# Performance work log

Measured on AMD Instinct MI355X. Metric: run time of the kernel, lower is better.

Reference implementation:

```python
import jax, jax.numpy as jnp
import numpy as np

N_CELL, N_TISSUE, H, NH = 200000, 2000, 256, 8
HD = H // NH
SCALE = HD ** -0.5
EPS = 1e-5


def _layernorm(x, g, b):
    m = jnp.mean(x, axis=-1, keepdims=True)
    v = jnp.mean((x - m) ** 2, axis=-1, keepdims=True)
    return (x - m) / jnp.sqrt(v + EPS) * g + b


def setup_inputs() -> dict:
    key = jax.random.key(0)
    ks = jax.random.split(key, 12)
    s = 0.02

    def lin(k):
        k1, k2 = jax.random.split(k)
        return (jax.random.normal(k1, (H, H), jnp.float32) * s,
                jax.random.normal(k2, (H,), jnp.float32) * s)

    Wq_bu, bq_bu = lin(ks[0])
    Wk_bu, bk_bu = lin(ks[1])
    Wv_bu, bv_bu = lin(ks[2])
    Wo_bu, bo_bu = lin(ks[3])
    Wv_td, bv_td = lin(ks[4])
    Wo_td, bo_td = lin(ks[5])
    return dict(
        cell_features=jax.random.normal(ks[6], (N_CELL, H), jnp.float32),
        tissue_features=jax.random.normal(ks[7], (N_TISSUE, H), jnp.float32),
        cluster_labels=jax.random.randint(ks[8], (N_CELL,), 0, N_TISSUE, dtype=jnp.int32),
        tissue_batch=jnp.zeros((N_TISSUE,), jnp.int32),
        Wq_bu=Wq_bu, bq_bu=bq_bu, Wk_bu=Wk_bu, bk_bu=bk_bu,
        Wv_bu=Wv_bu, bv_bu=bv_bu, Wo_bu=Wo_bu, bo_bu=bo_bu,
        Wv_td=Wv_td, bv_td=bv_td, Wo_td=Wo_td, bo_td=bo_td,
        ln_cell_g=jnp.ones((H,), jnp.float32), ln_cell_b=jnp.zeros((H,), jnp.float32),
        ln_tissue_g=jnp.ones((H,), jnp.float32), ln_tissue_b=jnp.zeros((H,), jnp.float32),
    )


def reference(cell_features, tissue_features, cluster_labels, tissue_batch,
              Wq_bu, bq_bu, Wk_bu, bk_bu, Wv_bu, bv_bu, Wo_bu, bo_bu,
              Wv_td, bv_td, Wo_td, bo_td,
              ln_cell_g, ln_cell_b, ln_tissue_g, ln_tissue_b):
    Nc = cell_features.shape[0]
    Nt = tissue_features.shape[0]

    # ---- bottom-up: each tissue node (1 query) attends over its cells (segment attention) ----
    Q = (tissue_features @ Wq_bu + bq_bu).reshape(Nt, NH, HD)   # [Nt, h, d]
    K = (cell_features @ Wk_bu + bk_bu).reshape(Nc, NH, HD)     # [Nc, h, d]
    V = (cell_features @ Wv_bu + bv_bu).reshape(Nc, NH, HD)     # [Nc, h, d]

    # per-cell score against its own cluster's tissue query
    scores = jnp.einsum('nhd,nhd->nh', K, Q[cluster_labels]) * SCALE  # [Nc, h]
    smax = jax.lax.stop_gradient(
        jax.ops.segment_max(scores, cluster_labels, num_segments=Nt))  # [Nt, h]
    ex = jnp.exp(scores - smax[cluster_labels])
    denom = jax.ops.segment_sum(ex, cluster_labels, num_segments=Nt)   # [Nt, h]
    w = ex / denom[cluster_labels]                                     # [Nc, h]
    attended = jax.ops.segment_sum(w[..., None] * V, cluster_labels,
                                   num_segments=Nt)                    # [Nt, h, d]
    attended = attended.reshape(Nt, H) @ Wo_bu + bo_bu

    counts = jax.ops.segment_sum(jnp.ones((Nc,), cell_features.dtype),
                                 cluster_labels, num_segments=Nt)
    tissue_updated = jnp.where(counts[:, None] > 0, attended, tissue_features)

    # ---- top-down: each cell attends to its single tissue token ----
    # softmax over a single key is identically 1, so q/k projections cancel:
    # attended_cell = out_proj(v_proj(tissue_updated[cluster]))
    td_per_tissue = (tissue_updated @ Wv_td + bv_td) @ Wo_td + bo_td   # [Nt, H]
    cell_updated = td_per_tissue[cluster_labels]                       # [Nc, H]

    cell_out = _layernorm(cell_features + cell_updated, ln_cell_g, ln_cell_b)
    tissue_out = _layernorm(tissue_features + tissue_updated, ln_tissue_g, ln_tissue_b)
    return (cell_out, tissue_out)
```

## Files before the change

### kernel.cpp

```cpp
#include <hip/hip_runtime.h>
#include <math.h>

#define NC 200000
#define NT 2000
#define HH 256
#define NH_ 8
#define SCALE 0.17677669529663687f
#define EPS 1e-5f
#define SLICE 128
#define PSLICES (NT + NC / SLICE + 1)
#define PSTRIDE 2056


__global__ void k_hist(const int* __restrict__ labels, int* __restrict__ counts) {
  int i = blockIdx.x * 256 + threadIdx.x;
  if (i < NC) atomicAdd(&counts[labels[i]], 1);
}

__global__ void k_scan(const int* __restrict__ counts, int* __restrict__ offsets,
                       int* __restrict__ soff, int* __restrict__ slice_t) {
  int tid = threadIdx.x;
  int base = tid * 32;
  int la[32], lb[32], scnt[32];
  int sa = 0, sb = 0;
  #pragma unroll
  for (int k = 0; k < 32; k++) {
    int idx = base + k;
    int v = (idx < NT) ? counts[idx] : 0;
    la[k] = sa; lb[k] = sb;
    scnt[k] = (v + SLICE - 1) / SLICE;
    sa += v; sb += scnt[k];
  }
  int ia_ = sa, ib_ = sb;
  #pragma unroll
  for (int d = 1; d < 64; d <<= 1) {
    int oa = __shfl_up(ia_, d, 64);
    int ob = __shfl_up(ib_, d, 64);
    if (tid >= d) { ia_ += oa; ib_ += ob; }
  }
  int ea = ia_ - sa, eb = ib_ - sb;
  #pragma unroll
  for (int k = 0; k < 32; k++) {
    int idx = base + k;
    if (idx < NT) {
      offsets[idx] = ea + la[k];
      soff[idx] = eb + lb[k];
      int st = eb + lb[k];
      for (int s2 = 0; s2 < scnt[k]; s2++) slice_t[st + s2] = idx;
    }
  }
  if (tid == 63) { offsets[NT] = ia_; soff[NT] = ib_; }
}

__global__ void k_scatter(const int* __restrict__ labels, const int* __restrict__ offsets,
                          int* __restrict__ cursor, int* __restrict__ cindex) {
  int i = blockIdx.x * 256 + threadIdx.x;
  if (i < NC) {
    int c = labels[i];
    int pos = offsets[c] + atomicAdd(&cursor[c], 1);
    cindex[pos] = i;
  }
}


__global__ __launch_bounds__(256) void k_gemm_bias(
    const float* __restrict__ A, const float* __restrict__ W,
    const float* __restrict__ bias, float* __restrict__ C, int M)
{
  __shared__ float Al[16][33];
  __shared__ float Wl[32][HH];
  int tid = threadIdx.x;
  int r0 = blockIdx.x * 16;
  float acc[16];
  #pragma unroll
  for (int r = 0; r < 16; r++) acc[r] = 0.f;
  for (int k0 = 0; k0 < HH; k0 += 32) {
    for (int e = tid; e < 16 * 32; e += 256) {
      int r = e >> 5, k = e & 31;
      int row = r0 + r;
      Al[r][k] = (row < M) ? A[(size_t)row * HH + k0 + k] : 0.f;
    }
    for (int e = tid; e < 32 * HH; e += 256) {
      int k = e >> 8, j = e & 255;
      Wl[k][j] = W[(size_t)(k0 + k) * HH + j];
    }
    __syncthreads();
    for (int k = 0; k < 32; k++) {
      float w = Wl[k][tid];
      #pragma unroll
      for (int r = 0; r < 16; r++) acc[r] += Al[r][k] * w;
    }
    __syncthreads();
  }
  float bj = bias[tid];
  #pragma unroll
  for (int r = 0; r < 16; r++) {
    int row = r0 + r;
    if (row < M) C[(size_t)row * HH + tid] = acc[r] + bj;
  }
}


__global__ __launch_bounds__(256) void k_qproj(
    const float* __restrict__ Q, const float* __restrict__ Wk,
    const float* __restrict__ bk, float* __restrict__ Qproj,
    float* __restrict__ bkq)
{
  __shared__ float Al[64][33];
  __shared__ float Bl[32][257];
  int h = blockIdx.x & 7, tb = blockIdx.x >> 3;
  int t0 = tb * 64;
  int tid = threadIdx.x;
  for (int e = tid; e < 64 * 32; e += 256) {
    int r = e >> 5, d = e & 31;
    int t = t0 + r;
    Al[r][d] = (t < NT) ? Q[(size_t)t * HH + h * 32 + d] * SCALE : 0.f;
  }
  for (int e = tid; e < 256 * 32; e += 256) {
    int j = e >> 5, d = e & 31;
    Bl[d][j] = Wk[(size_t)j * HH + h * 32 + d];
  }
  __syncthreads();
  float acc[64];
  #pragma unroll
  for (int r = 0; r < 64; r++) acc[r] = 0.f;
  for (int d = 0; d < 32; d++) {
    float b = Bl[d][tid];
    #pragma unroll
    for (int r = 0; r < 64; r++) acc[r] += Al[r][d] * b;
  }
  for (int r = 0; r < 64; r++) {
    int t = t0 + r;
    if (t < NT) Qproj[((size_t)t * NH_ + h) * HH + tid] = acc[r];
  }
  if (tid < 64) {
    int t = t0 + tid;
    if (t < NT) {
      float s = 0.f;
      #pragma unroll
      for (int d = 0; d < 32; d++) s += Al[tid][d] * bk[h * 32 + d];
      bkq[t * NH_ + h] = s;
    }
  }
}


#define GRP 4
#define ROWF 260

__global__ __launch_bounds__(256) void k_cellslice(
    const float* __restrict__ cell, const int* __restrict__ cindex,
    const int* __restrict__ offsets, const int* __restrict__ soff,
    const int* __restrict__ slice_t,
    const float* __restrict__ Qproj, const float* __restrict__ bkq,
    float* __restrict__ Pbuf)
{
  __shared__ int   cidx[SLICE];
  __shared__ float xbuf[4][GRP][ROWF];
  __shared__ float cwlds[NH_][HH];
  __shared__ float red[4][NH_];

  int s = blockIdx.x;
  if (s >= soff[NT]) return;
  int t = slice_t[s];
  int l = s - soff[t];
  int c0 = offsets[t] + l * SLICE;
  int c1 = min(c0 + SLICE, offsets[t + 1]);
  int nc = c1 - c0;

  int tid = threadIdx.x;
  int w = tid >> 6, lane = tid & 63;
  int hg = lane & 3, kc = lane >> 2;

  if (tid < SLICE) cidx[tid] = cindex[min(c0 + tid, c1 - 1)];

  const float* qpb = Qproj + (size_t)t * NH_ * HH;
  float4 qp0[4], qp1[4];
  #pragma unroll
  for (int i = 0; i < 4; i++) {
    qp0[i] = *reinterpret_cast<const float4*>(qpb + (2 * hg) * HH + (i * 16 + kc) * 4);
    qp1[i] = *reinterpret_cast<const float4*>(qpb + (2 * hg + 1) * HH + (i * 16 + kc) * 4);
  }
  float bq0 = bkq[t * NH_ + 2 * hg];
  float bq1 = bkq[t * NH_ + 2 * hg + 1];

  float4 cw0[4], cw1[4];
  #pragma unroll
  for (int i = 0; i < 4; i++) {
    cw0[i] = make_float4(0.f, 0.f, 0.f, 0.f);
    cw1[i] = make_float4(0.f, 0.f, 0.f, 0.f);
  }
  float d0 = 0.f, d1 = 0.f;

  __syncthreads();

  float (*myx)[ROWF] = xbuf[w];
  int base = w * GRP;
  float4 st[GRP];

  #pragma unroll
  for (int r = 0; r < GRP; r++)
    st[r] = *reinterpret_cast<const float4*>(
        &cell[(size_t)cidx[min(base + r, nc - 1)] * HH + lane * 4]);
  #pragma unroll
  for (int r = 0; r < GRP; r++)
    *reinterpret_cast<float4*>(&myx[r][lane * 4]) = st[r];

  for (int gb = base; gb < nc; gb += 16) {
    int gn = gb + 16;
    bool more = gn < nc;
    if (more) {
      #pragma unroll
      for (int r = 0; r < GRP; r++)
        st[r] = *reinterpret_cast<const float4*>(
            &cell[(size_t)cidx[min(gn + r, nc - 1)] * HH + lane * 4]);
    }
    #pragma unroll
    for (int c = 0; c < GRP; c++) {
      float4 x0 = *reinterpret_cast<float4*>(&myx[c][(0 * 16 + kc) * 4]);
      float4 x1 = *reinterpret_cast<float4*>(&myx[c][(1 * 16 + kc) * 4]);
      float4 x2 = *reinterpret_cast<float4*>(&myx[c][(2 * 16 + kc) * 4]);
      float4 x3 = *reinterpret_cast<float4*>(&myx[c][(3 * 16 + kc) * 4]);
      float s0 = x0.x * qp0[0].x + x0.y * qp0[0].y + x0.z * qp0[0].z + x0.w * qp0[0].w
               + x1.x * qp0[1].x + x1.y * qp0[1].y + x1.z * qp0[1].z + x1.w * qp0[1].w
               + x2.x * qp0[2].x + x2.y * qp0[2].y + x2.z * qp0[2].z + x2.w * qp0[2].w
               + x3.x * qp0[3].x + x3.y * qp0[3].y + x3.z * qp0[3].z + x3.w * qp0[3].w;
      float s1 = x0.x * qp1[0].x + x0.y * qp1[0].y + x0.z * qp1[0].z + x0.w * qp1[0].w
               + x1.x * qp1[1].x + x1.y * qp1[1].y + x1.z * qp1[1].z + x1.w * qp1[1].w
               + x2.x * qp1[2].x + x2.y * qp1[2].y + x2.z * qp1[2].z + x2.w * qp1[2].w
               + x3.x * qp1[3].x + x3.y * qp1[3].y + x3.z * qp1[3].z + x3.w * qp1[3].w;
      #pragma unroll
      for (int d = 4; d < 64; d <<= 1) {
        s0 += __shfl_xor(s0, d, 64);
        s1 += __shfl_xor(s1, d, 64);
      }
      float e0 = __expf(s0 + bq0);
      float e1 = __expf(s1 + bq1);
      if (gb + c >= nc) { e0 = 0.f; e1 = 0.f; }
      d0 += e0; d1 += e1;
      cw0[0].x += e0 * x0.x; cw0[0].y += e0 * x0.y; cw0[0].z += e0 * x0.z; cw0[0].w += e0 * x0.w;
      cw0[1].x += e0 * x1.x; cw0[1].y += e0 * x1.y; cw0[1].z += e0 * x1.z; cw0[1].w += e0 * x1.w;
      cw0[2].x += e0 * x2.x; cw0[2].y += e0 * x2.y; cw0[2].z += e0 * x2.z; cw0[2].w += e0 * x2.w;
      cw0[3].x += e0 * x3.x; cw0[3].y += e0 * x3.y; cw0[3].z += e0 * x3.z; cw0[3].w += e0 * x3.w;
      cw1[0].x += e1 * x0.x; cw1[0].y += e1 * x0.y; cw1[0].z += e1 * x0.z; cw1[0].w += e1 * x0.w;
      cw1[1].x += e1 * x1.x; cw1[1].y += e1 * x1.y; cw1[1].z += e1 * x1.z; cw1[1].w += e1 * x1.w;
      cw1[2].x += e1 * x2.x; cw1[2].y += e1 * x2.y; cw1[2].z += e1 * x2.z; cw1[2].w += e1 * x2.w;
      cw1[3].x += e1 * x3.x; cw1[3].y += e1 * x3.y; cw1[3].z += e1 * x3.z; cw1[3].w += e1 * x3.w;
    }
    if (more) {
      #pragma unroll
      for (int r = 0; r < GRP; r++)
        *reinterpret_cast<float4*>(&myx[r][lane * 4]) = st[r];
    }
  }

  if (w == 0) {
    #pragma unroll
    for (int i = 0; i < 4; i++) {
      *reinterpret_cast<float4*>(&cwlds[2 * hg][(i * 16 + kc) * 4]) = cw0[i];
      *reinterpret_cast<float4*>(&cwlds[2 * hg + 1][(i * 16 + kc) * 4]) = cw1[i];
    }
  }
  if (kc == 0) { red[w][2 * hg] = d0; red[w][2 * hg + 1] = d1; }
  __syncthreads();
  #pragma unroll
  for (int ww = 1; ww < 4; ww++) {
    if (w == ww) {
      #pragma unroll
      for (int i = 0; i < 4; i++) {
        float4 a = *reinterpret_cast<float4*>(&cwlds[2 * hg][(i * 16 + kc) * 4]);
        a.x += cw0[i].x; a.y += cw0[i].y; a.z += cw0[i].z; a.w += cw0[i].w;
        *reinterpret_cast<float4*>(&cwlds[2 * hg][(i * 16 + kc) * 4]) = a;
        float4 b = *reinterpret_cast<float4*>(&cwlds[2 * hg + 1][(i * 16 + kc) * 4]);
        b.x += cw1[i].x; b.y += cw1[i].y; b.z += cw1[i].z; b.w += cw1[i].w;
        *reinterpret_cast<float4*>(&cwlds[2 * hg + 1][(i * 16 + kc) * 4]) = b;
      }
    }
    __syncthreads();
  }

  float* pb = Pbuf + (size_t)s * PSTRIDE;
  #pragma unroll
  for (int h = 0; h < NH_; h++) pb[h * HH + tid] = cwlds[h][tid];
  if (tid < NH_) pb[2048 + tid] = red[0][tid] + red[1][tid] + red[2][tid] + red[3][tid];
}


#define TCH 4

__global__ __launch_bounds__(256) void k_tissuechain(
    const float* __restrict__ tissue, const int* __restrict__ counts,
    const float* __restrict__ Pbuf, const int* __restrict__ soff,
    const float* __restrict__ Wv, const float* __restrict__ bv,
    const float* __restrict__ Wo, const float* __restrict__ bo,
    const float* __restrict__ Wvtd, const float* __restrict__ bvtd,
    const float* __restrict__ Wotd, const float* __restrict__ botd,
    const float* __restrict__ lng, const float* __restrict__ lnb,
    float* __restrict__ td, float* __restrict__ out_tissue)
{
  __shared__ float s_cwn[TCH][NH_ * HH];
  __shared__ float s_a[TCH][HH];
  __shared__ float s_tu[TCH][HH];
  __shared__ float s_tmp[TCH][HH];
  __shared__ float s_red[2][4];
  __shared__ float s_dinv[TCH][NH_];
  int t0 = blockIdx.x * TCH;
  int j = threadIdx.x;
  int h = j >> 5;

  if (j < TCH * NH_) {
    int t = j >> 3, hh = j & 7;
    int s0 = soff[t0 + t], s1 = soff[t0 + t + 1];
    float d = 0.f;
    for (int q = s0; q < s1; q++) d += Pbuf[(size_t)q * PSTRIDE + 2048 + hh];
    s_dinv[t][hh] = (s1 > s0) ? 1.f / d : 0.f;
  }
  __syncthreads();

  for (int e = j; e < TCH * NH_ * HH; e += 256) {
    int t = e >> 11, c = e & 2047, hh = c >> 8;
    int s0 = soff[t0 + t], s1 = soff[t0 + t + 1];
    float a = 0.f;
    for (int q = s0; q < s1; q++) a += Pbuf[(size_t)q * PSTRIDE + c];
    s_cwn[t][c] = a * s_dinv[t][hh];
  }
  __syncthreads();

  float acc[TCH];
  #pragma unroll
  for (int t = 0; t < TCH; t++) acc[t] = 0.f;
  for (int k = 0; k < HH; k++) {
    float w = Wv[(size_t)k * HH + j];
    #pragma unroll
    for (int t = 0; t < TCH; t++) acc[t] += s_cwn[t][h * HH + k] * w;
  }
  {
    float bj = bv[j];
    #pragma unroll
    for (int t = 0; t < TCH; t++) s_a[t][j] = acc[t] + bj;
  }
  __syncthreads();

  #pragma unroll
  for (int t = 0; t < TCH; t++) acc[t] = 0.f;
  for (int k = 0; k < HH; k++) {
    float w = Wo[(size_t)k * HH + j];
    #pragma unroll
    for (int t = 0; t < TCH; t++) acc[t] += s_a[t][k] * w;
  }
  {
    float bj = bo[j];
    #pragma unroll
    for (int t = 0; t < TCH; t++) {
      int tt = t0 + t;
      s_tu[t][j] = (counts[tt] > 0) ? (acc[t] + bj) : tissue[(size_t)tt * HH + j];
    }
  }
  __syncthreads();

  #pragma unroll
  for (int t = 0; t < TCH; t++) acc[t] = 0.f;
  for (int k = 0; k < HH; k++) {
    float w = Wvtd[(size_t)k * HH + j];
    #pragma unroll
    for (int t = 0; t < TCH; t++) acc[t] += s_tu[t][k] * w;
  }
  {
    float bj = bvtd[j];
    #pragma unroll
    for (int t = 0; t < TCH; t++) s_tmp[t][j] = acc[t] + bj;
  }
  __syncthreads();

  #pragma unroll
  for (int t = 0; t < TCH; t++) acc[t] = 0.f;
  for (int k = 0; k < HH; k++) {
    float w = Wotd[(size_t)k * HH + j];
    #pragma unroll
    for (int t = 0; t < TCH; t++) acc[t] += s_tmp[t][k] * w;
  }
  {
    float bj = botd[j];
    #pragma unroll
    for (int t = 0; t < TCH; t++) td[(size_t)(t0 + t) * HH + j] = acc[t] + bj;
  }

  float gj = lng[j], bj2 = lnb[j];
  for (int t = 0; t < TCH; t++) {
    float y = tissue[(size_t)(t0 + t) * HH + j] + s_tu[t][j];
    float s1 = y, s2 = y * y;
    #pragma unroll
    for (int d = 1; d < 64; d <<= 1) { s1 += __shfl_xor(s1, d, 64); s2 += __shfl_xor(s2, d, 64); }
    int wv_ = j >> 6, ln_ = j & 63;
    __syncthreads();
    if (ln_ == 0) { s_red[0][wv_] = s1; s_red[1][wv_] = s2; }
    __syncthreads();
    s1 = s_red[0][0] + s_red[0][1] + s_red[0][2] + s_red[0][3];
    s2 = s_red[1][0] + s_red[1][1] + s_red[1][2] + s_red[1][3];
    float mean = s1 * (1.f / 256.f);
    float var = s2 * (1.f / 256.f) - mean * mean;
    float inv = rsqrtf(var + EPS);
    out_tissue[(size_t)(t0 + t) * HH + j] = (y - mean) * inv * gj + bj2;
  }
}


#define COB 4096

__global__ __launch_bounds__(256) void k_cellout(
    const float* __restrict__ cell, const float* __restrict__ td,
    const int* __restrict__ labels,
    const float* __restrict__ lng, const float* __restrict__ lnb,
    float* __restrict__ out)
{
  int lane = threadIdx.x & 63;
  float4 gv = *reinterpret_cast<const float4*>(&lng[lane * 4]);
  float4 bvv = *reinterpret_cast<const float4*>(&lnb[lane * 4]);
  const int stride = COB * 4;
  int wid = blockIdx.x * 4 + (threadIdx.x >> 6);
  for (int row = wid; row < NC; row += 2 * stride) {
    int rowB = row + stride;
    bool hasB = rowB < NC;
    int cA = labels[row];
    float4 xA = *reinterpret_cast<const float4*>(&cell[(size_t)row * HH + lane * 4]);
    float4 uA = *reinterpret_cast<const float4*>(&td[(size_t)cA * HH + lane * 4]);
    float4 xB, uB;
    if (hasB) {
      int cB = labels[rowB];
      xB = *reinterpret_cast<const float4*>(&cell[(size_t)rowB * HH + lane * 4]);
      uB = *reinterpret_cast<const float4*>(&td[(size_t)cB * HH + lane * 4]);
    }
    {
      float y0 = xA.x + uA.x, y1 = xA.y + uA.y, y2 = xA.z + uA.z, y3 = xA.w + uA.w;
      float s1 = y0 + y1 + y2 + y3;
      float s2 = y0 * y0 + y1 * y1 + y2 * y2 + y3 * y3;
      #pragma unroll
      for (int d = 1; d < 64; d <<= 1) { s1 += __shfl_xor(s1, d, 64); s2 += __shfl_xor(s2, d, 64); }
      float mean = s1 * (1.f / 256.f);
      float var = s2 * (1.f / 256.f) - mean * mean;
      float inv = rsqrtf(var + EPS);
      float4 o;
      o.x = (y0 - mean) * inv * gv.x + bvv.x;
      o.y = (y1 - mean) * inv * gv.y + bvv.y;
      o.z = (y2 - mean) * inv * gv.z + bvv.z;
      o.w = (y3 - mean) * inv * gv.w + bvv.w;
      *reinterpret_cast<float4*>(&out[(size_t)row * HH + lane * 4]) = o;
    }
    if (hasB) {
      float y0 = xB.x + uB.x, y1 = xB.y + uB.y, y2 = xB.z + uB.z, y3 = xB.w + uB.w;
      float s1 = y0 + y1 + y2 + y3;
      float s2 = y0 * y0 + y1 * y1 + y2 * y2 + y3 * y3;
      #pragma unroll
      for (int d = 1; d < 64; d <<= 1) { s1 += __shfl_xor(s1, d, 64); s2 += __shfl_xor(s2, d, 64); }
      float mean = s1 * (1.f / 256.f);
      float var = s2 * (1.f / 256.f) - mean * mean;
      float inv = rsqrtf(var + EPS);
      float4 o;
      o.x = (y0 - mean) * inv * gv.x + bvv.x;
      o.y = (y1 - mean) * inv * gv.y + bvv.y;
      o.z = (y2 - mean) * inv * gv.z + bvv.z;
      o.w = (y3 - mean) * inv * gv.w + bvv.w;
      *reinterpret_cast<float4*>(&out[(size_t)rowB * HH + lane * 4]) = o;
    }
  }
}


extern "C" void kernel_launch(void* const* d_in, const int* in_sizes, int n_in,
                              void* d_out, int out_size, void* d_ws, size_t ws_size,
                              hipStream_t stream) {
  const float* cell   = (const float*)d_in[0];
  const float* tissue = (const float*)d_in[1];
  const int*   labels = (const int*)d_in[2];
  const float* Wq = (const float*)d_in[4];  const float* bq = (const float*)d_in[5];
  const float* Wk = (const float*)d_in[6];  const float* bk = (const float*)d_in[7];
  const float* Wv = (const float*)d_in[8];  const float* bv = (const float*)d_in[9];
  const float* Wo = (const float*)d_in[10]; const float* bo = (const float*)d_in[11];
  const float* Wvtd = (const float*)d_in[12]; const float* bvtd = (const float*)d_in[13];
  const float* Wotd = (const float*)d_in[14]; const float* botd = (const float*)d_in[15];
  const float* lncg = (const float*)d_in[16]; const float* lncb = (const float*)d_in[17];
  const float* lntg = (const float*)d_in[18]; const float* lntb = (const float*)d_in[19];
  float* out_cell   = (float*)d_out;
  float* out_tissue = (float*)d_out + (size_t)NC * HH;

  char* w = (char*)d_ws;
  auto take = [&](size_t bytes) { void* p = (void*)w; w += (bytes + 255) & ~(size_t)255; return p; };
  int*   counts  = (int*)take((size_t)NT * 4);
  int*   cursor  = (int*)take((size_t)NT * 4);
  int*   offsets = (int*)take((size_t)(NT + 1) * 4);
  int*   soff    = (int*)take((size_t)(NT + 1) * 4);
  int*   slice_t = (int*)take((size_t)PSLICES * 4);
  int*   cindex  = (int*)take((size_t)NC * 4);
  float* Q       = (float*)take((size_t)NT * HH * 4);
  float* Qproj   = (float*)take((size_t)NT * NH_ * HH * 4);
  float* bkq     = (float*)take((size_t)NT * NH_ * 4);
  float* td      = (float*)take((size_t)NT * HH * 4);
  float* Pbuf    = (float*)take((size_t)PSLICES * PSTRIDE * 4);

  hipMemsetAsync(counts, 0, 16384, stream);

  const int CB = (NC + 255) / 256;
  k_hist<<<CB, 256, 0, stream>>>(labels, counts);
  k_scan<<<1, 64, 0, stream>>>(counts, offsets, soff, slice_t);
  k_scatter<<<CB, 256, 0, stream>>>(labels, offsets, cursor, cindex);

  k_gemm_bias<<<(NT + 15) / 16, 256, 0, stream>>>(tissue, Wq, bq, Q, NT);
  k_qproj<<<8 * ((NT + 63) / 64), 256, 0, stream>>>(Q, Wk, bk, Qproj, bkq);

  k_cellslice<<<PSLICES, 256, 0, stream>>>(cell, cindex, offsets, soff, slice_t,
                                           Qproj, bkq, Pbuf);

  k_tissuechain<<<NT / TCH, 256, 0, stream>>>(tissue, counts, Pbuf, soff,
      Wv, bv, Wo, bo, Wvtd, bvtd, Wotd, botd, lntg, lntb, td, out_tissue);

  k_cellout<<<COB, 256, 0, stream>>>(cell, td, labels, lncg, lncb, out_cell);
}
```

Measured before the change: 441.8 us.

## Sort cells into a contiguous bf16 copy and stream it in cellslice

The scatter kernel now writes a bf16-packed copy of each cell row into cluster-sorted order, so k_cellslice reads contiguous half-width rows straight into registers instead of gathering fp32 rows by index through shared memory. The goal is to replace the indirect fp32 gather with a coalesced read of half the bytes and to drop the LDS staging. The cost is an extra full pass over the cell features (a 200k x 256 fp32 read plus a bf16 write), and the attention math now runs on bf16-rounded inputs, which lowers accuracy.

```diff
diff --git a/kernel.cpp b/kernel.cpp
--- a/kernel.cpp
+++ b/kernel.cpp
@@ -52,13 +52,38 @@
   if (tid == 63) { offsets[NT] = ia_; soff[NT] = ib_; }
 }
 
-__global__ void k_scatter(const int* __restrict__ labels, const int* __restrict__ offsets,
-                          int* __restrict__ cursor, int* __restrict__ cindex) {
-  int i = blockIdx.x * 256 + threadIdx.x;
-  if (i < NC) {
-    int c = labels[i];
-    int pos = offsets[c] + atomicAdd(&cursor[c], 1);
-    cindex[pos] = i;
+
+__device__ inline unsigned pk2(float a, float b) {
+  unsigned ua = (__float_as_uint(a) + 0x8000u) >> 16;
+  unsigned ub = (__float_as_uint(b) + 0x8000u) & 0xFFFF0000u;
+  return ua | ub;
+}
+__device__ inline float lo16(unsigned u) { return __uint_as_float(u << 16); }
+__device__ inline float hi16(unsigned u) { return __uint_as_float(u & 0xFFFF0000u); }
+
+
+#define SCVB 2048
+
+__global__ __launch_bounds__(256) void k_sortcvt(
+    const float* __restrict__ cell, const int* __restrict__ labels,
+    const int* __restrict__ offsets, int* __restrict__ cursor,
+    unsigned short* __restrict__ cellb)
+{
+  int lane = threadIdx.x & 63;
+  int w = blockIdx.x * 4 + (threadIdx.x >> 6);
+  const int nw = SCVB * 4;
+  for (int i = w; i < NC; i += nw) {
+    int pos = 0;
+    if (lane == 0) {
+      int c = labels[i];
+      pos = offsets[c] + atomicAdd(&cursor[c], 1);
+    }
+    pos = __shfl(pos, 0, 64);
+    float4 x = *reinterpret_cast<const float4*>(&cell[(size_t)i * HH + lane * 4]);
+    uint2 o;
+    o.x = pk2(x.x, x.y);
+    o.y = pk2(x.z, x.w);
+    *reinterpret_cast<uint2*>(&cellb[(size_t)pos * HH + lane * 4]) = o;
   }
 }
 
@@ -145,18 +170,13 @@
 }
 
 
-#define GRP 4
-#define ROWF 260
-
 __global__ __launch_bounds__(256) void k_cellslice(
-    const float* __restrict__ cell, const int* __restrict__ cindex,
+    const unsigned short* __restrict__ cellb,
     const int* __restrict__ offsets, const int* __restrict__ soff,
     const int* __restrict__ slice_t,
     const float* __restrict__ Qproj, const float* __restrict__ bkq,
     float* __restrict__ Pbuf)
 {
-  __shared__ int   cidx[SLICE];
-  __shared__ float xbuf[4][GRP][ROWF];
   __shared__ float cwlds[NH_][HH];
   __shared__ float red[4][NH_];
 
@@ -172,8 +192,6 @@
   int w = tid >> 6, lane = tid & 63;
   int hg = lane & 3, kc = lane >> 2;
 
-  if (tid < SLICE) cidx[tid] = cindex[min(c0 + tid, c1 - 1)];
-
   const float* qpb = Qproj + (size_t)t * NH_ * HH;
   float4 qp0[4], qp1[4];
   #pragma unroll
@@ -192,66 +210,47 @@
   }
   float d0 = 0.f, d1 = 0.f;
 
-  __syncthreads();
-
-  float (*myx)[ROWF] = xbuf[w];
-  int base = w * GRP;
-  float4 st[GRP];
-
-  #pragma unroll
-  for (int r = 0; r < GRP; r++)
-    st[r] = *reinterpret_cast<const float4*>(
-        &cell[(size_t)cidx[min(base + r, nc - 1)] * HH + lane * 4]);
-  #pragma unroll
-  for (int r = 0; r < GRP; r++)
-    *reinterpret_cast<float4*>(&myx[r][lane * 4]) = st[r];
-
-  for (int gb = base; gb < nc; gb += 16) {
-    int gn = gb + 16;
-    bool more = gn < nc;
-    if (more) {
-      #pragma unroll
-      for (int r = 0; r < GRP; r++)
-        st[r] = *reinterpret_cast<const float4*>(
-            &cell[(size_t)cidx[min(gn + r, nc - 1)] * HH + lane * 4]);
-    }
-    #pragma unroll
-    for (int c = 0; c < GRP; c++) {
-      float4 x0 = *reinterpret_cast<float4*>(&myx[c][(0 * 16 + kc) * 4]);
-      float4 x1 = *reinterpret_cast<float4*>(&myx[c][(1 * 16 + kc) * 4]);
-      float4 x2 = *reinterpret_cast<float4*>(&myx[c][(2 * 16 + kc) * 4]);
-      float4 x3 = *reinterpret_cast<float4*>(&myx[c][(3 * 16 + kc) * 4]);
-      float s0 = x0.x * qp0[0].x + x0.y * qp0[0].y + x0.z * qp0[0].z + x0.w * qp0[0].w
-               + x1.x * qp0[1].x + x1.y * qp0[1].y + x1.z * qp0[1].z + x1.w * qp0[1].w
-               + x2.x * qp0[2].x + x2.y * qp0[2].y + x2.z * qp0[2].z + x2.w * qp0[2].w
-               + x3.x * qp0[3].x + x3.y * qp0[3].y + x3.z * qp0[3].z + x3.w * qp0[3].w;
-      float s1 = x0.x * qp1[0].x + x0.y * qp1[0].y + x0.z * qp1[0].z + x0.w * qp1[0].w
-               + x1.x * qp1[1].x + x1.y * qp1[1].y + x1.z * qp1[1].z + x1.w * qp1[1].w
-               + x2.x * qp1[2].x + x2.y * qp1[2].y + x2.z * qp1[2].z + x2.w * qp1[2].w
-               + x3.x * qp1[3].x + x3.y * qp1[3].y + x3.z * qp1[3].z + x3.w * qp1[3].w;
-      #pragma unroll
-      for (int d = 4; d < 64; d <<= 1) {
-        s0 += __shfl_xor(s0, d, 64);
-        s1 += __shfl_xor(s1, d, 64);
-      }
-      float e0 = __expf(s0 + bq0);
-      float e1 = __expf(s1 + bq1);
-      if (gb + c >= nc) { e0 = 0.f; e1 = 0.f; }
-      d0 += e0; d1 += e1;
-      cw0[0].x += e0 * x0.x; cw0[0].y += e0 * x0.y; cw0[0].z += e0 * x0.z; cw0[0].w += e0 * x0.w;
-      cw0[1].x += e0 * x1.x; cw0[1].y += e0 * x1.y; cw0[1].z += e0 * x1.z; cw0[1].w += e0 * x1.w;
-      cw0[2].x += e0 * x2.x; cw0[2].y += e0 * x2.y; cw0[2].z += e0 * x2.z; cw0[2].w += e0 * x2.w;
-      cw0[3].x += e0 * x3.x; cw0[3].y += e0 * x3.y; cw0[3].z += e0 * x3.z; cw0[3].w += e0 * x3.w;
-      cw1[0].x += e1 * x0.x; cw1[0].y += e1 * x0.y; cw1[0].z += e1 * x0.z; cw1[0].w += e1 * x0.w;
-      cw1[1].x += e1 * x1.x; cw1[1].y += e1 * x1.y; cw1[1].z += e1 * x1.z; cw1[1].w += e1 * x1.w;
-      cw1[2].x += e1 * x2.x; cw1[2].y += e1 * x2.y; cw1[2].z += e1 * x2.z; cw1[2].w += e1 * x2.w;
-      cw1[3].x += e1 * x3.x; cw1[3].y += e1 * x3.y; cw1[3].z += e1 * x3.z; cw1[3].w += e1 * x3.w;
-    }
-    if (more) {
-      #pragma unroll
-      for (int r = 0; r < GRP; r++)
-        *reinterpret_cast<float4*>(&myx[r][lane * 4]) = st[r];
-    }
+  uint2 xv[4], nv[4];
+  {
+    const uint2* p = reinterpret_cast<const uint2*>(cellb + (size_t)(c0 + min(w, nc - 1)) * HH);
+    #pragma unroll
+    for (int i = 0; i < 4; i++) xv[i] = p[i * 16 + kc];
+  }
+
+  for (int ic = w; ic < nc; ic += 4) {
+    int icn = min(ic + 4, nc - 1);
+    const uint2* pn = reinterpret_cast<const uint2*>(cellb + (size_t)(c0 + icn) * HH);
+    #pragma unroll
+    for (int i = 0; i < 4; i++) nv[i] = pn[i * 16 + kc];
+
+    float4 x[4];
+    #pragma unroll
+    for (int i = 0; i < 4; i++)
+      x[i] = make_float4(lo16(xv[i].x), hi16(xv[i].x), lo16(xv[i].y), hi16(xv[i].y));
+
+    float s0 = 0.f, s1 = 0.f;
+    #pragma unroll
+    for (int i = 0; i < 4; i++) {
+      s0 += x[i].x * qp0[i].x + x[i].y * qp0[i].y + x[i].z * qp0[i].z + x[i].w * qp0[i].w;
+      s1 += x[i].x * qp1[i].x + x[i].y * qp1[i].y + x[i].z * qp1[i].z + x[i].w * qp1[i].w;
+    }
+    #pragma unroll
+    for (int d = 4; d < 64; d <<= 1) {
+      s0 += __shfl_xor(s0, d, 64);
+      s1 += __shfl_xor(s1, d, 64);
+    }
+    float e0 = __expf(s0 + bq0);
+    float e1 = __expf(s1 + bq1);
+    d0 += e0; d1 += e1;
+    #pragma unroll
+    for (int i = 0; i < 4; i++) {
+      cw0[i].x += e0 * x[i].x; cw0[i].y += e0 * x[i].y;
+      cw0[i].z += e0 * x[i].z; cw0[i].w += e0 * x[i].w;
+      cw1[i].x += e1 * x[i].x; cw1[i].y += e1 * x[i].y;
+      cw1[i].z += e1 * x[i].z; cw1[i].w += e1 * x[i].w;
+    }
+    #pragma unroll
+    for (int i = 0; i < 4; i++) xv[i] = nv[i];
   }
 
   if (w == 0) {
@@ -490,24 +489,24 @@
   int*   offsets = (int*)take((size_t)(NT + 1) * 4);
   int*   soff    = (int*)take((size_t)(NT + 1) * 4);
   int*   slice_t = (int*)take((size_t)PSLICES * 4);
-  int*   cindex  = (int*)take((size_t)NC * 4);
   float* Q       = (float*)take((size_t)NT * HH * 4);
   float* Qproj   = (float*)take((size_t)NT * NH_ * HH * 4);
   float* bkq     = (float*)take((size_t)NT * NH_ * 4);
   float* td      = (float*)take((size_t)NT * HH * 4);
   float* Pbuf    = (float*)take((size_t)PSLICES * PSTRIDE * 4);
+  unsigned short* cellb = (unsigned short*)take((size_t)NC * HH * 2);
 
   hipMemsetAsync(counts, 0, 16384, stream);
 
   const int CB = (NC + 255) / 256;
   k_hist<<<CB, 256, 0, stream>>>(labels, counts);
   k_scan<<<1, 64, 0, stream>>>(counts, offsets, soff, slice_t);
-  k_scatter<<<CB, 256, 0, stream>>>(labels, offsets, cursor, cindex);
+  k_sortcvt<<<SCVB, 256, 0, stream>>>(cell, labels, offsets, cursor, cellb);
 
   k_gemm_bias<<<(NT + 15) / 16, 256, 0, stream>>>(tissue, Wq, bq, Q, NT);
   k_qproj<<<8 * ((NT + 63) / 64), 256, 0, stream>>>(Q, Wk, bk, Qproj, bkq);
 
-  k_cellslice<<<PSLICES, 256, 0, stream>>>(cell, cindex, offsets, soff, slice_t,
+  k_cellslice<<<PSLICES, 256, 0, stream>>>(cellb, offsets, soff, slice_t,
                                            Qproj, bkq, Pbuf);
 
   k_tissuechain<<<NT / TCH, 256, 0, stream>>>(tissue, counts, Pbuf, soff,
```

Result: no change. 435.4 us (-1.5%).
